# Optimization experiments

Hardware: AMD Instinct MI355X
Metric: run time of the kernel (lower is better)

Reference implementation:

```python
import jax, jax.numpy as jnp
import numpy as np

B, N, D, H, E, ED = 32, 256, 1024, 16, 512, 256
HD = D // H
NEG = float(np.finfo(np.float32).min)


def setup_inputs() -> dict:
    key = jax.random.key(0)
    ks = iter(jax.random.split(key, 16))
    def nrm(shape, fan_in):
        return jax.random.normal(next(ks), shape, jnp.float32) / np.sqrt(fan_in)
    return {
        "x": jax.random.normal(next(ks), (B, N, D), jnp.float32),
        "node_masks": jnp.ones((B, N), jnp.float32),
        "relation_edges": jax.random.randint(next(ks), (B, E, 2), 0, N, jnp.int64),
        "relation_masks": jnp.ones((B, E), jnp.float32),
        "relation_embeddings": jax.random.normal(next(ks), (B, E, ED), jnp.float32),
        "ln_g": jnp.ones((D,), jnp.float32), "ln_b": jnp.zeros((D,), jnp.float32),
        "Wq": nrm((D, D), D), "bq": jnp.zeros((D,), jnp.float32),
        "Wk": nrm((D, D), D), "bk": jnp.zeros((D,), jnp.float32),
        "Wv": nrm((D, D), D), "bv": jnp.zeros((D,), jnp.float32),
        "We": nrm((ED, H), ED), "be": jnp.zeros((H,), jnp.float32),
        "Wo": nrm((D, D), D), "bo": jnp.zeros((D,), jnp.float32),
        "ff_g": jnp.ones((D,), jnp.float32), "ff_b": jnp.zeros((D,), jnp.float32),
        "W1": nrm((D, 4 * D), D), "b1": jnp.zeros((4 * D,), jnp.float32),
        "W2": nrm((4 * D, D), 4 * D), "b2": jnp.zeros((D,), jnp.float32),
    }


def _ln(x, g, b):
    m = jnp.mean(x, axis=-1, keepdims=True)
    v = jnp.mean((x - m) ** 2, axis=-1, keepdims=True)
    return (x - m) / jnp.sqrt(v + 1e-5) * g + b


def reference(x, node_masks, relation_edges, relation_masks, relation_embeddings,
              ln_g, ln_b, Wq, bq, Wk, bk, Wv, bv, We, be, Wo, bo,
              ff_g, ff_b, W1, b1, W2, b2):
    residual = x
    xn = _ln(x, ln_g, ln_b)
    # [B,N,D] -> [B,H,N,HD]
    def split_heads(t):
        return t.reshape(B, N, H, HD).transpose(0, 2, 1, 3)
    q = split_heads(xn @ Wq + bq)
    k = split_heads(xn @ Wk + bk)
    v = split_heads(xn @ Wv + bv)
    attn = jnp.einsum('bhqd,bhkd->bhqk', q, k) / np.sqrt(HD)

    nb = node_masks.astype(bool)
    pair_mask = nb[:, None, :, None] & nb[:, None, None, :]  # [B,1,N,N]

    # --- scatter edge list into dense adjacency + per-head bias ---
    src = jnp.clip(relation_edges[..., 0], 0, N - 1)  # [B,E]
    dst = jnp.clip(relation_edges[..., 1], 0, N - 1)
    valid = relation_masks.astype(bool)
    # route invalid edges to a padding row/col N, sliced off afterwards
    src_w = jnp.where(valid, src, N)
    dst_w = jnp.where(valid, dst, N)
    b_idx = jnp.broadcast_to(jnp.arange(B)[:, None], (B, E))

    Np = N + 1
    adj = jnp.broadcast_to(jnp.eye(Np, dtype=bool), (B, Np, Np))
    adj = adj.at[b_idx, src_w, dst_w].set(True).at[b_idx, dst_w, src_w].set(True)
    rel_adj = adj[:, :N, :N][:, None]  # [B,1,N,N]

    eb = relation_embeddings @ We + be  # [B,E,H]
    bias = jnp.zeros((B, Np, Np, H), x.dtype)
    bias = bias.at[b_idx, src_w, dst_w].set(eb).at[b_idx, dst_w, src_w].set(eb)
    rel_bias = bias[:, :N, :N, :].transpose(0, 3, 1, 2)  # [B,H,N,N]

    attn = attn + rel_bias
    pair_mask = pair_mask & rel_adj
    attn = jnp.where(pair_mask, attn, NEG)
    attn = jax.nn.softmax(attn, axis=-1)
    attn = jnp.nan_to_num(attn)

    out = jnp.einsum('bhqk,bhkd->bhqd', attn, v).transpose(0, 2, 1, 3).reshape(B, N, D)
    x = residual + (out @ Wo + bo)
    h = _ln(x, ff_g, ff_b)
    h = jax.nn.silu(h @ W1 + b1) @ W2 + b2
    x = x + h
    return x * node_masks[..., None]
```

## Files before the change

### kernel.cpp

```cpp
#include <hip/hip_runtime.h>
#include <math.h>

#define B_  32
#define N_  256
#define D_  1024
#define H_  16
#define E_  512
#define ED_ 256
#define HD_ 64
#define QS_ 3072
#define NEG_ (-3.4028234663852886e38f)

typedef __attribute__((ext_vector_type(8))) short short8;
typedef __attribute__((ext_vector_type(4))) float f32x4;
typedef __attribute__((ext_vector_type(16))) float f32x16;
typedef unsigned short ushort_t;
typedef unsigned int uint_t;

union U16x8 { uint4 u4; ushort_t s[8]; };

static __device__ __forceinline__ ushort_t f2bf(float f) {
    uint_t u = __builtin_bit_cast(uint_t, f);
    u = (u + 0x7fff + ((u >> 16) & 1)) >> 16;
    return (ushort_t)u;
}

static __device__ __forceinline__ void gload_lds16(const void* g, void* l) {
    __builtin_amdgcn_global_load_lds(
        (const __attribute__((address_space(1))) unsigned int*)g,
        (__attribute__((address_space(3))) unsigned int*)l, 16, 0, 0);
}

__global__ __launch_bounds__(256) void ln_bf16_kernel(const float* __restrict__ x,
                                                      const float* __restrict__ g,
                                                      const float* __restrict__ b,
                                                      ushort_t* __restrict__ out) {
    int row = blockIdx.x;
    const float* xr = x + (size_t)row * D_;
    ushort_t* yr = out + (size_t)row * D_;
    __shared__ float red[256];
    int t = threadIdx.x;
    float vals[4];
    float s = 0.f;
#pragma unroll
    for (int i = 0; i < 4; ++i) { vals[i] = xr[t + i * 256]; s += vals[i]; }
    red[t] = s; __syncthreads();
    for (int off = 128; off > 0; off >>= 1) { if (t < off) red[t] += red[t + off]; __syncthreads(); }
    float mean = red[0] * (1.f / D_);
    __syncthreads();
    float vs = 0.f;
#pragma unroll
    for (int i = 0; i < 4; ++i) { float d = vals[i] - mean; vs += d * d; }
    red[t] = vs; __syncthreads();
    for (int off = 128; off > 0; off >>= 1) { if (t < off) red[t] += red[t + off]; __syncthreads(); }
    float rstd = 1.f / sqrtf(red[0] * (1.f / D_) + 1e-5f);
#pragma unroll
    for (int i = 0; i < 4; ++i) {
        int c = t + i * 256;
        yr[c] = f2bf((vals[i] - mean) * rstd * g[c] + b[c]);
    }
}

__global__ __launch_bounds__(256) void prep_kernel(
    const float* __restrict__ Wq, const float* __restrict__ Wk,
    const float* __restrict__ Wv, const float* __restrict__ Wo,
    const float* __restrict__ W1, const float* __restrict__ W2,
    const float* __restrict__ bq, const float* __restrict__ bk,
    const float* __restrict__ bv,
    ushort_t* __restrict__ qkvT, ushort_t* __restrict__ WoT,
    ushort_t* __restrict__ W1T, ushort_t* __restrict__ W2T,
    float* __restrict__ cb)
{
    int id = blockIdx.x;
    if (id >= 12288) {
        int i = (id - 12288) * 256 + threadIdx.x;
        cb[i] = (i < 1024) ? bq[i] : ((i < 2048) ? bk[i - 1024] : bv[i - 2048]);
        return;
    }
    const float* in; ushort_t* outp; int K, N, tid;
    if (id < 4096) {
        int wsel = id >> 10; tid = id & 1023; K = D_; N = D_;
        in   = (wsel == 0) ? Wq : (wsel == 1) ? Wk : (wsel == 2) ? Wv : Wo;
        outp = (wsel == 0) ? qkvT : (wsel == 1) ? qkvT + 1024 * 1024
             : (wsel == 2) ? qkvT + 2 * 1024 * 1024 : WoT;
    } else if (id < 8192) { tid = id - 4096; K = D_; N = 4 * D_; in = W1; outp = W1T; }
    else                  { tid = id - 8192; K = 4 * D_; N = D_; in = W2; outp = W2T; }
    int tilesX = N >> 5;
    int n0 = (tid % tilesX) * 32, k0 = (tid / tilesX) * 32;

    __shared__ float tile[32][33];
    int tx = threadIdx.x & 31, ty = threadIdx.x >> 5;
#pragma unroll
    for (int r = 0; r < 4; ++r)
        tile[ty + r * 8][tx] = in[(size_t)(k0 + ty + r * 8) * N + n0 + tx];
    __syncthreads();
#pragma unroll
    for (int r = 0; r < 4; ++r)
        outp[(size_t)(n0 + ty + r * 8) * K + k0 + tx] = f2bf(tile[tx][ty + r * 8]);
}

__global__ __launch_bounds__(256) void eb_kernel(const float* __restrict__ re,
                                                 const float* __restrict__ We,
                                                 const float* __restrict__ be,
                                                 float* __restrict__ eb) {
    __shared__ float rs[16 * 256];
    __shared__ float wl[256 * 16];
    int t = threadIdx.x;
    int be0 = blockIdx.x * 16;
#pragma unroll
    for (int i = 0; i < 16; ++i) wl[t + i * 256] = We[t + i * 256];
#pragma unroll
    for (int i = 0; i < 16; ++i) rs[t + i * 256] = re[(size_t)be0 * 256 + t + i * 256];
    __syncthreads();
    int el = t >> 4, h = t & 15;
    float s = be[h];
#pragma unroll 8
    for (int i = 0; i < 256; ++i) s += rs[el * 256 + i] * wl[i * 16 + h];
    eb[(size_t)(be0 + el) * 16 + h] = s;
}

__global__ void scatter_kernel(const int* __restrict__ edges, const float* __restrict__ emask,
                               int* __restrict__ prio) {
    int idx = blockIdx.x * blockDim.x + threadIdx.x;
    if (idx >= B_ * E_) return;
    if (emask[idx] == 0.f) return;
    int b = idx / E_, e = idx % E_;
    int s = edges[2 * idx], d = edges[2 * idx + 1];
    s = min(max(s, 0), N_ - 1);
    d = min(max(d, 0), N_ - 1);
    int* base = prio + (size_t)b * N_ * N_;
    atomicMax(&base[s * N_ + d], e);
    atomicMax(&base[d * N_ + s], e + E_);
}

template<int MODE>
__global__ __launch_bounds__(256) void gemm_bf16(
    const ushort_t* __restrict__ A, const ushort_t* __restrict__ BT,
    const float* __restrict__ bias, const float* __restrict__ res,
    const float* __restrict__ nm, void* __restrict__ Cout,
    int M, int N, int K)
{
    __shared__ ushort_t As[128 * 64];
    __shared__ ushort_t Bs[128 * 64];
    int t = threadIdx.x;
    int lane = t & 63;
    int l31 = lane & 31, lh = lane >> 5;
    int w = t >> 6;
    int wr = (w >> 1) * 64, wc = (w & 1) * 64;

    int bid = blockIdx.x;
    int xcd = bid & 7;
    int lid = bid >> 3;
    int st  = lid >> 5;
    int ls  = lid & 31;
    int brow = xcd * 8 + (ls >> 2);
    int bcol = st * 4 + (ls & 3);
    int row0 = brow * 128, col0 = bcol * 128;

    const ushort_t* Ag = A + (size_t)row0 * K;
    const ushort_t* Bg = BT + (size_t)col0 * K;
    int srow = t >> 3;
    int slot = t & 7;
    int sc = (slot ^ (srow & 7)) * 8;

    f32x16 acc[2][2];
#pragma unroll
    for (int i = 0; i < 2; ++i)
#pragma unroll
        for (int j = 0; j < 2; ++j)
#pragma unroll
            for (int r = 0; r < 16; ++r) acc[i][j][r] = 0.f;

    for (int k0 = 0; k0 < K; k0 += 64) {
#pragma unroll
        for (int i = 0; i < 4; ++i) {
            gload_lds16(Ag + (size_t)(i * 32 + srow) * K + k0 + sc, (char*)As + i * 4096 + t * 16);
            gload_lds16(Bg + (size_t)(i * 32 + srow) * K + k0 + sc, (char*)Bs + i * 4096 + t * 16);
        }
        __syncthreads();
#pragma unroll
        for (int ks = 0; ks < 4; ++ks) {
            short8 af[2], bfr[2];
#pragma unroll
            for (int it = 0; it < 2; ++it) {
                int m = wr + it * 32 + l31;
                int x = ((ks * 2 + lh) ^ (m & 7)) * 16;
                af[it] = *(const short8*)((const char*)As + m * 128 + x);
            }
#pragma unroll
            for (int jt = 0; jt < 2; ++jt) {
                int n = wc + jt * 32 + l31;
                int x = ((ks * 2 + lh) ^ (n & 7)) * 16;
                bfr[jt] = *(const short8*)((const char*)Bs + n * 128 + x);
            }
#pragma unroll
            for (int it = 0; it < 2; ++it)
#pragma unroll
                for (int jt = 0; jt < 2; ++jt)
                    acc[it][jt] = __builtin_amdgcn_mfma_f32_32x32x16_bf16(af[it], bfr[jt], acc[it][jt], 0, 0, 0);
        }
        __syncthreads();
    }

#pragma unroll
    for (int it = 0; it < 2; ++it) {
#pragma unroll
        for (int jt = 0; jt < 2; ++jt) {
            int col = col0 + wc + jt * 32 + l31;
            float bcol_b = bias[col];
#pragma unroll
            for (int reg = 0; reg < 16; ++reg) {
                int row = row0 + wr + it * 32 + (reg & 3) + 8 * (reg >> 2) + 4 * lh;
                float v = acc[it][jt][reg] + bcol_b;
                if (MODE == 0) {
                    ((ushort_t*)Cout)[(size_t)row * N + col] = f2bf(v);
                } else {
                    v = v / (1.f + __expf(-v));
                    ((ushort_t*)Cout)[(size_t)row * N + col] = f2bf(v);
                }
            }
        }
    }
}

template<int MODE>
__global__ __launch_bounds__(256) void gemm_res(
    const ushort_t* __restrict__ A, const ushort_t* __restrict__ BT,
    const float* __restrict__ bias, const float* __restrict__ res,
    const float* __restrict__ nm, void* __restrict__ Cout,
    int M, int N, int K)
{
    __shared__ ushort_t As[2][128 * 64];
    __shared__ ushort_t Bs[2][128 * 64];
    int t = threadIdx.x;
    int lane = t & 63;
    int l31 = lane & 31, lh = lane >> 5;
    int w = t >> 6;
    int wr = (w >> 1) * 64, wc = (w & 1) * 64;

    int bid = blockIdx.x;
    int xcd = bid & 7;
    int lid = bid >> 3;
    int st  = lid >> 5;
    int ls  = lid & 31;
    int brow = xcd * 8 + (ls >> 2);
    int bcol = st * 4 + (ls & 3);
    int row0 = brow * 128, col0 = bcol * 128;

    const ushort_t* Ag = A + (size_t)row0 * K;
    const ushort_t* Bg = BT + (size_t)col0 * K;
    int srow = t >> 3;
    int slot = t & 7;
    int sc = (slot ^ (srow & 7)) * 8;

    f32x16 acc[2][2];
#pragma unroll
    for (int i = 0; i < 2; ++i)
#pragma unroll
        for (int j = 0; j < 2; ++j)
#pragma unroll
            for (int r = 0; r < 16; ++r) acc[i][j][r] = 0.f;

    for (int k0 = 0; k0 < K; k0 += 128) {
#pragma unroll
        for (int p = 0; p < 2; ++p)
#pragma unroll
            for (int i = 0; i < 4; ++i) {
                gload_lds16(Ag + (size_t)(i * 32 + srow) * K + k0 + p * 64 + sc,
                            (char*)As + p * 16384 + i * 4096 + t * 16);
                gload_lds16(Bg + (size_t)(i * 32 + srow) * K + k0 + p * 64 + sc,
                            (char*)Bs + p * 16384 + i * 4096 + t * 16);
            }
        __syncthreads();
#pragma unroll
        for (int ks8 = 0; ks8 < 8; ++ks8) {
            const char* Ab = (const char*)As + (ks8 >> 2) * 16384;
            const char* Bb = (const char*)Bs + (ks8 >> 2) * 16384;
            int kk = ks8 & 3;
            short8 af[2], bfr[2];
#pragma unroll
            for (int it = 0; it < 2; ++it) {
                int m = wr + it * 32 + l31;
                int x = ((kk * 2 + lh) ^ (m & 7)) * 16;
                af[it] = *(const short8*)(Ab + m * 128 + x);
            }
#pragma unroll
            for (int jt = 0; jt < 2; ++jt) {
                int n = wc + jt * 32 + l31;
                int x = ((kk * 2 + lh) ^ (n & 7)) * 16;
                bfr[jt] = *(const short8*)(Bb + n * 128 + x);
            }
#pragma unroll
            for (int it = 0; it < 2; ++it)
#pragma unroll
                for (int jt = 0; jt < 2; ++jt)
                    acc[it][jt] = __builtin_amdgcn_mfma_f32_32x32x16_bf16(af[it], bfr[jt], acc[it][jt], 0, 0, 0);
        }
        __syncthreads();
    }

#pragma unroll
    for (int it = 0; it < 2; ++it) {
#pragma unroll
        for (int jt = 0; jt < 2; ++jt) {
            int col = col0 + wc + jt * 32 + l31;
            float bcol_b = bias[col];
#pragma unroll
            for (int reg = 0; reg < 16; ++reg) {
                int row = row0 + wr + it * 32 + (reg & 3) + 8 * (reg >> 2) + 4 * lh;
                float v = acc[it][jt][reg] + bcol_b;
                if (MODE == 1) {
                    ((float*)Cout)[(size_t)row * N + col] = v + res[(size_t)row * N + col];
                } else {
                    v = (v + res[(size_t)row * N + col]) * nm[row];
                    ((float*)Cout)[(size_t)row * N + col] = v;
                }
            }
        }
    }
}

__global__ __launch_bounds__(256, 2) void attn_mfma_kernel(
    const ushort_t* __restrict__ qkv, const int* __restrict__ prio,
    const float* __restrict__ eb, const float* __restrict__ nm,
    ushort_t* __restrict__ out)
{
    int xb = blockIdx.x;
    int bid = (xb & 7) * 256 + (xb >> 3);
    int h = bid & 15, qt = (bid >> 4) & 3, b = bid >> 6;
    int t = threadIdx.x;

    __shared__ ushort_t Ks[256 * 72];
    __shared__ ushort_t Vt[64 * 264];

    int lane = t & 63, c = lane & 15, quad = lane >> 4;
    int w = t >> 6;
    int qbase = qt * 64 + w * 16 + quad * 4;

    int pr[16][4];
    const int* prp = prio + ((size_t)(b * N_ + qbase)) * N_ + c;
#pragma unroll
    for (int j = 0; j < 16; ++j)
#pragma unroll
        for (int r = 0; r < 4; ++r)
            pr[j][r] = prp[(size_t)r * N_ + j * 16];

    float nmq[4];
#pragma unroll
    for (int r = 0; r < 4; ++r) nmq[r] = nm[b * N_ + qbase + r];
    float nmk[16];
#pragma unroll
    for (int j = 0; j < 16; ++j) nmk[j] = nm[b * N_ + j * 16 + c];

    const ushort_t* qg = qkv + ((size_t)(b * N_ + qt * 64 + w * 16 + c)) * QS_ + h * HD_;
    short8 aq0 = *(const short8*)(const void*)(qg + quad * 8);
    short8 aq1 = *(const short8*)(const void*)(qg + 32 + quad * 8);

    int lr = t >> 3, lc = (t & 7) * 8;
    const ushort_t* kg = qkv + ((size_t)(b * N_)) * QS_ + 1024 + h * HD_;
#pragma unroll
    for (int r = 0; r < 256; r += 32)
        *(uint4*)&Ks[(lr + r) * 72 + lc] = *(const uint4*)&kg[(size_t)(lr + r) * QS_ + lc];
    const ushort_t* vg = qkv + ((size_t)(b * N_)) * QS_ + 2048 + h * HD_;
#pragma unroll
    for (int r = 0; r < 256; r += 32) {
        U16x8 uu; uu.u4 = *(const uint4*)&vg[(size_t)(lr + r) * QS_ + lc];
#pragma unroll
        for (int i = 0; i < 8; ++i)
            Vt[(lc + i) * 264 + lr + r] = uu.s[i];
    }

    const float* ebb = eb + (size_t)b * E_ * H_ + h;
    float badd[16][4];
#pragma unroll
    for (int j = 0; j < 16; ++j) {
        int key = j * 16 + c;
#pragma unroll
        for (int r = 0; r < 4; ++r) {
            int p = pr[j][r];
            float bias = 0.f;
            bool adj = (key == qbase + r);
            if (p >= 0) {
                int e = (p >= E_) ? p - E_ : p;
                bias = ebb[(size_t)e * H_];
                adj = true;
            }
            bool ok = adj && (nmq[r] != 0.f) && (nmk[j] != 0.f);
            badd[j][r] = ok ? bias : -3.0e38f;
        }
    }
    __syncthreads();

    f32x4 z = {0.f, 0.f, 0.f, 0.f};
    f32x4 acc[16];
#pragma unroll
    for (int j = 0; j < 16; ++j) acc[j] = z;
    __builtin_amdgcn_s_setprio(1);
#pragma unroll
    for (int j = 0; j < 16; ++j) {
        short8 b0 = *(const short8*)(const void*)(Ks + (j * 16 + c) * 72 + quad * 8);
        short8 b1 = *(const short8*)(const void*)(Ks + (j * 16 + c) * 72 + 32 + quad * 8);
        acc[j] = __builtin_amdgcn_mfma_f32_16x16x32_bf16(aq0, b0, acc[j], 0, 0, 0);
        acc[j] = __builtin_amdgcn_mfma_f32_16x16x32_bf16(aq1, b1, acc[j], 0, 0, 0);
    }
    __builtin_amdgcn_s_setprio(0);

#pragma unroll
    for (int j = 0; j < 16; ++j)
#pragma unroll
        for (int r = 0; r < 4; ++r)
            acc[j][r] = acc[j][r] * 0.125f + badd[j][r];

    float inv[4];
#pragma unroll
    for (int r = 0; r < 4; ++r) {
        float m = acc[0][r];
#pragma unroll
        for (int j = 1; j < 16; ++j) m = fmaxf(m, acc[j][r]);
        m = fmaxf(m, __shfl_xor(m, 1));
        m = fmaxf(m, __shfl_xor(m, 2));
        m = fmaxf(m, __shfl_xor(m, 4));
        m = fmaxf(m, __shfl_xor(m, 8));
        float s = 0.f;
#pragma unroll
        for (int j = 0; j < 16; ++j) {
            float p = __expf(acc[j][r] - m);
            acc[j][r] = p;
            s += p;
        }
        s += __shfl_xor(s, 1);
        s += __shfl_xor(s, 2);
        s += __shfl_xor(s, 4);
        s += __shfl_xor(s, 8);
        inv[r] = 1.f / s;
    }

    __syncthreads();
    ushort_t* Ps = Ks;
#pragma unroll
    for (int j = 0; j < 16; ++j)
#pragma unroll
        for (int r = 0; r < 4; ++r)
            Ps[(w * 16 + quad * 4 + r) * 264 + j * 16 + c] = f2bf(acc[j][r] * inv[r]);
    asm volatile("s_waitcnt lgkmcnt(0)" ::: "memory");

    f32x4 oc[4];
#pragma unroll
    for (int dt = 0; dt < 4; ++dt) oc[dt] = z;
    __builtin_amdgcn_s_setprio(1);
#pragma unroll
    for (int k0 = 0; k0 < 256; k0 += 32) {
        short8 ap = *(const short8*)(const void*)(Ps + (w * 16 + c) * 264 + k0 + quad * 8);
#pragma unroll
        for (int dt = 0; dt < 4; ++dt) {
            short8 bv = *(const short8*)(const void*)(Vt + (dt * 16 + c) * 264 + k0 + quad * 8);
            oc[dt] = __builtin_amdgcn_mfma_f32_16x16x32_bf16(ap, bv, oc[dt], 0, 0, 0);
        }
    }
    __builtin_amdgcn_s_setprio(0);
    ushort_t* og = out + ((size_t)(b * N_ + qt * 64 + w * 16)) * D_ + h * HD_;
#pragma unroll
    for (int dt = 0; dt < 4; ++dt)
#pragma unroll
        for (int r = 0; r < 4; ++r)
            og[(size_t)(quad * 4 + r) * D_ + dt * 16 + c] = f2bf(oc[dt][r]);
}

extern "C" void kernel_launch(void* const* d_in, const int* in_sizes, int n_in,
                              void* d_out, int out_size, void* d_ws, size_t ws_size,
                              hipStream_t stream) {
    const float* x     = (const float*)d_in[0];
    const float* nm    = (const float*)d_in[1];
    const int*   edges = (const int*)d_in[2];
    const float* emask = (const float*)d_in[3];
    const float* remb  = (const float*)d_in[4];
    const float* ln_g  = (const float*)d_in[5];
    const float* ln_b  = (const float*)d_in[6];
    const float* Wq = (const float*)d_in[7];  const float* bq = (const float*)d_in[8];
    const float* Wk = (const float*)d_in[9];  const float* bk = (const float*)d_in[10];
    const float* Wv = (const float*)d_in[11]; const float* bv = (const float*)d_in[12];
    const float* We = (const float*)d_in[13]; const float* be = (const float*)d_in[14];
    const float* Wo = (const float*)d_in[15]; const float* bo = (const float*)d_in[16];
    const float* ff_g = (const float*)d_in[17]; const float* ff_b = (const float*)d_in[18];
    const float* W1 = (const float*)d_in[19]; const float* b1 = (const float*)d_in[20];
    const float* W2 = (const float*)d_in[21]; const float* b2 = (const float*)d_in[22];
    float* out = (float*)d_out;

    char* ws = (char*)d_ws;
    const size_t MB = 1ll << 20;
    int*      prio = (int*)ws;
    float*    ebuf = (float*)(ws + 8 * MB);
    ushort_t* xn   = (ushort_t*)(ws + 9 * MB);
    float*    x2   = (float*)(ws + 25 * MB);
    ushort_t* hn   = (ushort_t*)(ws + 57 * MB);
    ushort_t* qkv  = (ushort_t*)(ws + 73 * MB);
    ushort_t* mid  = qkv;
    ushort_t* qkvT = (ushort_t*)(ws + 137 * MB);
    ushort_t* WoT  = (ushort_t*)(ws + 143 * MB);
    ushort_t* W1T  = (ushort_t*)(ws + 145 * MB);
    ushort_t* W2T  = (ushort_t*)(ws + 153 * MB);
    float*    cb   = (float*)(ws + 161 * MB);
    ushort_t* aout = xn;

    const int M = B_ * N_;

    (void)hipMemsetAsync(prio, 0xFF, (size_t)B_ * N_ * N_ * sizeof(int), stream);
    eb_kernel<<<B_ * E_ / 16, 256, 0, stream>>>(remb, We, be, ebuf);
    scatter_kernel<<<(B_ * E_ + 255) / 256, 256, 0, stream>>>(edges, emask, prio);

    prep_kernel<<<12300, 256, 0, stream>>>(Wq, Wk, Wv, Wo, W1, W2, bq, bk, bv,
                                           qkvT, WoT, W1T, W2T, cb);

    ln_bf16_kernel<<<M, 256, 0, stream>>>(x, ln_g, ln_b, xn);

    gemm_bf16<0><<<24 * 64, 256, 0, stream>>>(xn, qkvT, cb, nullptr, nullptr, qkv, M, QS_, D_);

    attn_mfma_kernel<<<B_ * H_ * 4, 256, 0, stream>>>(qkv, prio, ebuf, nm, aout);

    gemm_res<1><<<8 * 64, 256, 0, stream>>>(aout, WoT, bo, x, nullptr, x2, M, D_, D_);
    ln_bf16_kernel<<<M, 256, 0, stream>>>(x2, ff_g, ff_b, hn);

    gemm_bf16<2><<<32 * 64, 256, 0, stream>>>(hn, W1T, b1, nullptr, nullptr, mid, M, 4 * D_, D_);
    gemm_res<3><<<8 * 64, 256, 0, stream>>>(mid, W2T, b2, x2, nm, out, M, D_, 4 * D_);
}
```

Baseline: 496.3 us.

## Add 256x256-tile pipelined bf16 GEMM kernel for the FFN up-projection

```diff
diff --git a/kernel.cpp b/kernel.cpp
--- a/kernel.cpp
+++ b/kernel.cpp
@@ -318,6 +318,125 @@
             }
         }
     }
+}
+
+template<int NBN>
+__global__ __launch_bounds__(512) void gemm256(
+    const ushort_t* __restrict__ A, const ushort_t* __restrict__ BT,
+    const float* __restrict__ bias, ushort_t* __restrict__ Cout,
+    int M, int N, int K)
+{
+    __shared__ ushort_t As[2][2][128 * 64];
+    __shared__ ushort_t Bs[2][2][128 * 64];
+
+    int t = threadIdx.x;
+    int lane = t & 63;
+    int w = t >> 6;
+    int wm = w >> 2, wn = w & 3;
+    int c2 = lane & 15, quad = lane >> 4;
+
+    int bid = blockIdx.x;
+    int xcd = bid & 7, lid = bid >> 3;
+    int brow = xcd * 4 + (lid & 3);
+    int bcol = lid >> 2;
+    int row0 = brow * 256, col0 = bcol * 256;
+
+    const ushort_t* Ag = A + (size_t)row0 * K;
+    const ushort_t* Bg = BT + (size_t)col0 * K;
+
+    int srow = t >> 3, slot = t & 7;
+    int sc = (slot ^ (srow & 7)) * 8;
+
+    auto stage = [&](int buf, int hh, int kt) {
+        const ushort_t* g = (hh < 2) ? Ag : Bg;
+        int h = hh & 1;
+        char* l = (hh < 2) ? (char*)&As[buf][h][0] : (char*)&Bs[buf][h][0];
+        gload_lds16(g + (size_t)(h * 128 + srow) * K + kt * 64 + sc, l + t * 16);
+        gload_lds16(g + (size_t)(h * 128 + 64 + srow) * K + kt * 64 + sc, l + 8192 + t * 16);
+    };
+
+    f32x4 acc[8][4];
+#pragma unroll
+    for (int a_ = 0; a_ < 8; ++a_)
+#pragma unroll
+        for (int b_ = 0; b_ < 4; ++b_)
+#pragma unroll
+            for (int r = 0; r < 4; ++r) acc[a_][b_][r] = 0.f;
+
+    int T = K >> 6;
+    stage(0, 0, 0); stage(0, 1, 0); stage(0, 2, 0); stage(0, 3, 0);
+    if (T > 1) { stage(1, 2, 1); stage(1, 3, 1); stage(1, 0, 1); }
+
+    const int bhalf = wn >> 1, bco = (wn & 1) * 64;
+
+    for (int tau = 0; tau < T; ++tau) {
+        int bc = tau & 1;
+        const char* Ab = (const char*)&As[bc][wm][0];
+        const char* Bb = (const char*)&Bs[bc][bhalf][0];
+        short8 bfr[4][2];
+#pragma unroll
+        for (int q = 0; q < 4; ++q) {
+            if (q == 0) {
+                if (tau == T - 1) asm volatile("s_waitcnt vmcnt(0)" ::: "memory");
+                else              asm volatile("s_waitcnt vmcnt(6)" ::: "memory");
+                __builtin_amdgcn_s_barrier();
+                __builtin_amdgcn_sched_barrier(0);
+            }
+            short8 afr[2][2];
+#pragma unroll
+            for (int it = 0; it < 2; ++it)
+#pragma unroll
+                for (int ks = 0; ks < 2; ++ks) {
+                    int fr = q * 32 + it * 16 + c2;
+                    afr[it][ks] = *(const short8*)(Ab + fr * 128 + (((ks * 4 + quad) ^ (fr & 7)) * 16));
+                }
+            if (q == 0) {
+#pragma unroll
+                for (int jt = 0; jt < 4; ++jt)
+#pragma unroll
+                    for (int ks = 0; ks < 2; ++ks) {
+                        int fr = bco + jt * 16 + c2;
+                        bfr[jt][ks] = *(const short8*)(Bb + fr * 128 + (((ks * 4 + quad) ^ (fr & 7)) * 16));
+                    }
+            }
+            if (q == 0) { if (tau + 1 < T) stage(bc ^ 1, 1, tau + 1); }
+            else if (tau + 2 < T) stage(bc, (q == 1) ? 2 : (q == 2) ? 3 : 0, tau + 2);
+
+            asm volatile("s_waitcnt lgkmcnt(0)" ::: "memory");
+            __builtin_amdgcn_sched_barrier(0);
+            __builtin_amdgcn_s_setprio(1);
+#pragma unroll
+            for (int it = 0; it < 2; ++it)
+#pragma unroll
+                for (int jt = 0; jt < 4; ++jt) {
+                    acc[q * 2 + it][jt] = __builtin_amdgcn_mfma_f32_16x16x32_bf16(
+                        afr[it][0], bfr[jt][0], acc[q * 2 + it][jt], 0, 0, 0);
+                    acc[q * 2 + it][jt] = __builtin_amdgcn_mfma_f32_16x16x32_bf16(
+                        afr[it][1], bfr[jt][1], acc[q * 2 + it][jt], 0, 0, 0);
+                }
+            __builtin_amdgcn_s_setprio(0);
+            __builtin_amdgcn_sched_barrier(0);
+            __builtin_amdgcn_s_barrier();
+        }
+    }
+
+#pragma unroll
+    for (int q = 0; q < 4; ++q)
+#pragma unroll
+        for (int it = 0; it < 2; ++it) {
+            int row = row0 + wm * 128 + q * 32 + it * 16 + quad * 4;
+#pragma unroll
+            for (int jt = 0; jt < 4; ++jt) {
+                int col = col0 + wn * 64 + jt * 16 + c2;
+                float bc_ = bias[col];
+#pragma unroll
+                for (int r = 0; r < 4; ++r) {
+                    float v = acc[q * 2 + it][jt][r] + bc_;
+                    v = v / (1.f + __expf(-v));
+                    Cout[(size_t)(row + r) * N + col] = f2bf(v);
+                }
+            }
+        }
 }
 
 __global__ __launch_bounds__(256, 2) void attn_mfma_kernel(
@@ -520,6 +639,6 @@
     gemm_res<1><<<8 * 64, 256, 0, stream>>>(aout, WoT, bo, x, nullptr, x2, M, D_, D_);
     ln_bf16_kernel<<<M, 256, 0, stream>>>(x2, ff_g, ff_b, hn);
 
-    gemm_bf16<2><<<32 * 64, 256, 0, stream>>>(hn, W1T, b1, nullptr, nullptr, mid, M, 4 * D_, D_);
+    gemm256<16><<<512, 512, 0, stream>>>(hn, W1T, b1, mid, M, 4 * D_, D_);
     gemm_res<3><<<8 * 64, 256, 0, stream>>>(mid, W2T, b2, x2, nm, out, M, D_, 4 * D_);
 }
```

Measured after the change: 483.6 us, median of 3. 2.5% less time.
